# Kernel optimization log

Measured on AMD Instinct MI355X. Metric: run time of the kernel, lower is better.

The kernel has to match this reference:

```python
import jax, jax.numpy as jnp
import numpy as np

B, T, E, H, V = 64, 512, 512, 1024, 32000


def setup_inputs() -> dict:
    key = jax.random.key(0)
    k1, k2, k3, k4, k5 = jax.random.split(key, 5)
    scale = 1.0 / np.sqrt(H)
    return {
        "source": jax.random.randint(k1, (B, T), 0, V),
        "emb_table": jax.random.normal(k2, (V, E), dtype=jnp.float32),
        "W_ih": jax.random.normal(k3, (E, 4 * H), dtype=jnp.float32) * scale,
        "W_hh": jax.random.normal(k4, (H, 4 * H), dtype=jnp.float32) * scale,
        "b": jax.random.normal(k5, (4 * H,), dtype=jnp.float32) * scale,
    }


def reference(source, emb_table, W_ih, W_hh, b):
    # Embedding lookup: [B, T, E]
    embedded = emb_table[source]
    batch = source.shape[0]
    hidden = W_hh.shape[0]
    h0 = jnp.zeros((batch, hidden), dtype=emb_table.dtype)
    c0 = jnp.zeros((batch, hidden), dtype=emb_table.dtype)

    # Sequential LSTM cell loop over timesteps, expressed as lax.scan.
    xs = jnp.swapaxes(embedded, 0, 1)  # [T, B, E]

    def step(carry, x_t):
        h, c = carry
        z = x_t @ W_ih + h @ W_hh + b  # [B, 4H]
        i, f, g, o = jnp.split(z, 4, axis=-1)
        i = jax.nn.sigmoid(i)
        f = jax.nn.sigmoid(f)
        g = jnp.tanh(g)
        o = jax.nn.sigmoid(o)
        c_new = f * c + i * g
        h_new = o * jnp.tanh(c_new)
        return (h_new, c_new), None

    (h_T, c_T), _ = jax.lax.scan(step, (h0, c0), xs)
    return h_T, c_T
```

## Files before the change

### kernel.cpp

```cpp
#include <hip/hip_runtime.h>
#include <hip/hip_bf16.h>

#define TT 512
#define BB 64
#define EE 512
#define HH 1024

typedef __attribute__((ext_vector_type(8))) short short8;
typedef __attribute__((ext_vector_type(4))) float f32x4;

#define WS_X     0
#define WS_WT    33554432
#define WS_HBUF  46137344
#define WS_FLAGS 46399488
#define WS_PROBE 48496640

static __device__ __forceinline__ unsigned short f2bf(float x) {
    unsigned int u = __float_as_uint(x);
    unsigned int r = (u + 0x7fffu + ((u >> 16) & 1u)) >> 16;
    return (unsigned short)r;
}

static __device__ __forceinline__ int fl_ld(const int* p) {
    return __hip_atomic_load(p, __ATOMIC_RELAXED, __HIP_MEMORY_SCOPE_AGENT);
}
static __device__ __forceinline__ void fl_st(int* p, int v) {
    __hip_atomic_store(p, v, __ATOMIC_RELAXED, __HIP_MEMORY_SCOPE_AGENT);
}
static __device__ __forceinline__ void h_st(unsigned int* p, unsigned int v) {
    __hip_atomic_store(p, v, __ATOMIC_RELAXED, __HIP_MEMORY_SCOPE_AGENT);
}
static __device__ __forceinline__ short8 h_ld16(const unsigned long long* p) {
    union { short8 v; unsigned long long q[2]; } u;
    u.q[0] = __hip_atomic_load(p,     __ATOMIC_RELAXED, __HIP_MEMORY_SCOPE_AGENT);
    u.q[1] = __hip_atomic_load(p + 1, __ATOMIC_RELAXED, __HIP_MEMORY_SCOPE_AGENT);
    return u.v;
}

__global__ void embed_k(const int* __restrict__ src, const float* __restrict__ emb,
                        unsigned short* __restrict__ X) {
    int idx  = blockIdx.x * 256 + threadIdx.x;
    int base = idx * 4;
    int t = base >> 15;
    int r = base & 32767;
    int b = r >> 9;
    int e = r & 511;
    int v = src[b * TT + t];
    float4 f = *(const float4*)(emb + (size_t)v * EE + e);
    ushort4 s;
    s.x = f2bf(f.x); s.y = f2bf(f.y); s.z = f2bf(f.z); s.w = f2bf(f.w);
    *(ushort4*)(X + base) = s;
}

__global__ void wprep_k(const float* __restrict__ Wih, const float* __restrict__ Whh,
                        unsigned short* __restrict__ Wt, int* __restrict__ probe) {
    const int bid = blockIdx.x;
    const int kk  = bid % 48;
    const int ct  = bid / 48;
    const int tid = threadIdx.x;

    if (bid == 0 && tid == 0) {
        int xcd;
        asm volatile("s_getreg_b32 %0, hwreg(HW_REG_XCC_ID)" : "=s"(xcd));
        int* pr = probe;
        asm volatile("global_store_dword %0, %1, off sc0"
                     :: "v"(pr), "v"(xcd) : "memory");
        int v;
        asm volatile("global_load_dword %0, %1, off sc0\n\ts_waitcnt vmcnt(0)"
                     : "=v"(v) : "v"(pr) : "memory");
        pr[1] = v;
    }

    const int k0 = kk * 32, c0 = ct * 16;
    __shared__ float tile[32][17];
    for (int e = tid; e < 512; e += 256) {
        int kr = e >> 4, cc = e & 15;
        int k = k0 + kr;
        float v = (k < EE) ? Wih[(size_t)k * 4096 + c0 + cc]
                           : Whh[(size_t)(k - EE) * 4096 + c0 + cc];
        tile[kr][cc] = v;
    }
    __syncthreads();
    for (int e = tid; e < 512; e += 256) {
        int lane = e >> 3, j = e & 7;
        float v = tile[(lane >> 4) * 8 + j][lane & 15];
        Wt[(size_t)bid * 512 + e] = f2bf(v);
    }
}

__global__ __launch_bounds__(256, 1) void lstm_k(
    const unsigned short* __restrict__ X,
    const unsigned short* __restrict__ Wt,
    const float* __restrict__ bias,
    unsigned short* __restrict__ hbuf,
    int* __restrict__ flags,
    float* __restrict__ out)
{
    const int g        = blockIdx.x;
    const int cg       = g & 63;
    const int rg       = g >> 6;
    const int row_base = rg * 16;
    const int ubase    = cg * 16;
    const int tid  = threadIdx.x;
    const int wave = tid >> 6;
    const int lane = tid & 63;
    const int lrow = lane & 15;
    const int quad = lane >> 4;

    __shared__ float zred[4][4][16][17];
    __shared__ float sbias[64];

    if (tid < 64) sbias[tid] = bias[(tid >> 4) * HH + ubase + (tid & 15)];

    short8 wr[12][4];
#pragma unroll
    for (int i = 0; i < 12; ++i) {
        const int kk = i * 4 + wave;
#pragma unroll
        for (int g4 = 0; g4 < 4; ++g4) {
            const int ct = g4 * 64 + cg;
            wr[i][g4] = *(const short8*)(Wt + ((size_t)(ct * 48 + kk)) * 512 + lane * 8);
        }
    }

    const int erow = tid >> 4, eu = tid & 15;
    float creg = 0.f;
    __syncthreads();

    for (int t = 0; t < TT; ++t) {
        f32x4 acc0 = {0.f,0.f,0.f,0.f}, acc1 = {0.f,0.f,0.f,0.f};
        f32x4 acc2 = {0.f,0.f,0.f,0.f}, acc3 = {0.f,0.f,0.f,0.f};

        const unsigned short* xp = X + ((size_t)(t * BB) + row_base + lrow) * EE + quad * 8;
#pragma unroll
        for (int i = 0; i < 4; ++i) {
            const int kk = i * 4 + wave;
            short8 a = *(const short8*)(xp + kk * 32);
            acc0 = __builtin_amdgcn_mfma_f32_16x16x32_bf16(a, wr[i][0], acc0, 0, 0, 0);
            acc1 = __builtin_amdgcn_mfma_f32_16x16x32_bf16(a, wr[i][1], acc1, 0, 0, 0);
            acc2 = __builtin_amdgcn_mfma_f32_16x16x32_bf16(a, wr[i][2], acc2, 0, 0, 0);
            acc3 = __builtin_amdgcn_mfma_f32_16x16x32_bf16(a, wr[i][3], acc3, 0, 0, 0);
        }

        if (t > 0) {
            if (tid < 64) {
                const int* fp = &flags[(((t - 1) * 4 + rg) * 64 + tid) * 4];
                while (fl_ld(fp) == 0) { }
            }
            __syncthreads();
        }

        const unsigned long long* hq = (const unsigned long long*)hbuf
            + ((size_t)(((t & 1) ^ 1) * BB) + row_base + lrow) * (HH / 4) + quad * 2;
        short8 ah[8];
#pragma unroll
        for (int i = 0; i < 8; ++i) {
            const int kk = (i + 4) * 4 + wave;
            ah[i] = h_ld16(hq + (kk * 8 - 128));
        }
#pragma unroll
        for (int i = 0; i < 8; ++i) {
            acc0 = __builtin_amdgcn_mfma_f32_16x16x32_bf16(ah[i], wr[i + 4][0], acc0, 0, 0, 0);
            acc1 = __builtin_amdgcn_mfma_f32_16x16x32_bf16(ah[i], wr[i + 4][1], acc1, 0, 0, 0);
            acc2 = __builtin_amdgcn_mfma_f32_16x16x32_bf16(ah[i], wr[i + 4][2], acc2, 0, 0, 0);
            acc3 = __builtin_amdgcn_mfma_f32_16x16x32_bf16(ah[i], wr[i + 4][3], acc3, 0, 0, 0);
        }

#pragma unroll
        for (int r = 0; r < 4; ++r) {
            zred[wave][0][quad * 4 + r][lrow] = acc0[r];
            zred[wave][1][quad * 4 + r][lrow] = acc1[r];
            zred[wave][2][quad * 4 + r][lrow] = acc2[r];
            zred[wave][3][quad * 4 + r][lrow] = acc3[r];
        }
        __syncthreads();

        {
            float zi = zred[0][0][erow][eu] + zred[1][0][erow][eu]
                     + zred[2][0][erow][eu] + zred[3][0][erow][eu] + sbias[eu];
            float zf = zred[0][1][erow][eu] + zred[1][1][erow][eu]
                     + zred[2][1][erow][eu] + zred[3][1][erow][eu] + sbias[16 + eu];
            float zg = zred[0][2][erow][eu] + zred[1][2][erow][eu]
                     + zred[2][2][erow][eu] + zred[3][2][erow][eu] + sbias[32 + eu];
            float zo = zred[0][3][erow][eu] + zred[1][3][erow][eu]
                     + zred[2][3][erow][eu] + zred[3][3][erow][eu] + sbias[48 + eu];
            float iv = 1.f / (1.f + __expf(-zi));
            float fv = 1.f / (1.f + __expf(-zf));
            float gv = 1.f - 2.f / (__expf(2.f * zg) + 1.f);
            float ov = 1.f / (1.f + __expf(-zo));
            float c  = fv * creg + iv * gv;
            creg = c;
            float th = 1.f - 2.f / (__expf(2.f * c) + 1.f);
            float h  = ov * th;

            float hp = __shfl_xor(h, 1);
            if ((eu & 1) == 0) {
                unsigned int v = (unsigned int)f2bf(h)
                               | ((unsigned int)f2bf(hp) << 16);
                unsigned int* hw = (unsigned int*)hbuf;
                h_st(hw + ((size_t)(t & 1) * BB + row_base + erow) * (HH / 2)
                        + (ubase >> 1) + (eu >> 1), v);
            }
            if (t == TT - 1) {
                out[(row_base + erow) * HH + ubase + eu] = h;
                out[BB * HH + (row_base + erow) * HH + ubase + eu] = c;
            }
        }
        __syncthreads();

        if (tid == 0) {
            fl_st(&flags[((t * 4 + rg) * 64 + cg) * 4], 1);
        }
    }
}

extern "C" void kernel_launch(void* const* d_in, const int* in_sizes, int n_in,
                              void* d_out, int out_size, void* d_ws, size_t ws_size,
                              hipStream_t stream) {
    const int*   src  = (const int*)d_in[0];
    const float* emb  = (const float*)d_in[1];
    const float* Wih  = (const float*)d_in[2];
    const float* Whh  = (const float*)d_in[3];
    const float* bias = (const float*)d_in[4];
    float* out = (float*)d_out;

    char* ws = (char*)d_ws;
    unsigned short* X     = (unsigned short*)(ws + WS_X);
    unsigned short* Wt    = (unsigned short*)(ws + WS_WT);
    unsigned short* hbuf  = (unsigned short*)(ws + WS_HBUF);
    int*            flags = (int*)(ws + WS_FLAGS);
    int*            probe = (int*)(ws + WS_PROBE);

    hipMemsetAsync(hbuf, 0, 2 * BB * HH * 2, stream);
    hipMemsetAsync(flags, 0, TT * 4 * 64 * 4 * 4, stream);
    embed_k<<<dim3(16384), dim3(256), 0, stream>>>(src, emb, X);
    wprep_k<<<dim3(12288), dim3(256), 0, stream>>>(Wih, Whh, Wt, probe);
    lstm_k<<<dim3(256), dim3(256), 0, stream>>>(X, Wt, bias, hbuf, flags, out);
}
```

Baseline: 2.041 ms.

## Prefetch next-step inputs, vectorize h exchange, and spin-wait in every wave

The next timestep's x rows are prefetched with raw global loads after the cell update, so their latency overlaps the flag wait. The h state is now read with dwordx4 loads and written as 16-byte stores packed through lane shuffles, using sc0 sc1 cache bypass instead of atomic 8-byte and 4-byte accesses. Every wave now polls the flags itself with s_sleep, which removes a block barrier. Bias moves into registers and the __syncthreads calls become raw s_barrier with manual waitcnt. This shortens the per-step critical path of the recurrent loop, but memory ordering now depends on hand-placed waitcnt and cache bits, which is fragile.

```diff
diff --git a/kernel.cpp b/kernel.cpp
--- a/kernel.cpp
+++ b/kernel.cpp
@@ -8,6 +8,7 @@
 
 typedef __attribute__((ext_vector_type(8))) short short8;
 typedef __attribute__((ext_vector_type(4))) float f32x4;
+typedef __attribute__((ext_vector_type(4))) unsigned int u32x4;
 
 #define WS_X     0
 #define WS_WT    33554432
@@ -26,15 +27,6 @@
 }
 static __device__ __forceinline__ void fl_st(int* p, int v) {
     __hip_atomic_store(p, v, __ATOMIC_RELAXED, __HIP_MEMORY_SCOPE_AGENT);
-}
-static __device__ __forceinline__ void h_st(unsigned int* p, unsigned int v) {
-    __hip_atomic_store(p, v, __ATOMIC_RELAXED, __HIP_MEMORY_SCOPE_AGENT);
-}
-static __device__ __forceinline__ short8 h_ld16(const unsigned long long* p) {
-    union { short8 v; unsigned long long q[2]; } u;
-    u.q[0] = __hip_atomic_load(p,     __ATOMIC_RELAXED, __HIP_MEMORY_SCOPE_AGENT);
-    u.q[1] = __hip_atomic_load(p + 1, __ATOMIC_RELAXED, __HIP_MEMORY_SCOPE_AGENT);
-    return u.v;
 }
 
 __global__ void embed_k(const int* __restrict__ src, const float* __restrict__ emb,
@@ -106,11 +98,14 @@
     const int lane = tid & 63;
     const int lrow = lane & 15;
     const int quad = lane >> 4;
+    const int erow = tid >> 4, eu = tid & 15;
 
     __shared__ float zred[4][4][16][17];
-    __shared__ float sbias[64];
-
-    if (tid < 64) sbias[tid] = bias[(tid >> 4) * HH + ubase + (tid & 15)];
+
+    const float bi_ = bias[          ubase + eu];
+    const float bf_ = bias[HH      + ubase + eu];
+    const float bg_ = bias[2 * HH  + ubase + eu];
+    const float bo_ = bias[3 * HH  + ubase + eu];
 
     short8 wr[12][4];
 #pragma unroll
@@ -123,41 +118,51 @@
         }
     }
 
-    const int erow = tid >> 4, eu = tid & 15;
     float creg = 0.f;
-    __syncthreads();
+
+    short8 ax[4];
+    {
+        const unsigned short* xp = X + ((size_t)row_base + lrow) * EE + quad * 8;
+#pragma unroll
+        for (int i = 0; i < 4; ++i)
+            asm volatile("global_load_dwordx4 %0, %1, off"
+                         : "=v"(ax[i]) : "v"(xp + (i * 4 + wave) * 32) : "memory");
+    }
 
     for (int t = 0; t < TT; ++t) {
+        if (t > 0) {
+            const int* fp = &flags[(((t - 1) * 4 + rg) << 8) + (lane << 2)];
+            while (fl_ld(fp) == 0) { __builtin_amdgcn_s_sleep(1); }
+            asm volatile("s_waitcnt vmcnt(0)" ::: "memory");
+            __builtin_amdgcn_sched_barrier(0);
+        }
+
+        const unsigned short* hrow = hbuf
+            + ((size_t)(((t & 1) ^ 1) * BB) + row_base + lrow) * HH + quad * 8;
+        short8 ah[8];
+#pragma unroll
+        for (int i = 0; i < 8; ++i)
+            asm volatile("global_load_dwordx4 %0, %1, off sc0 sc1"
+                         : "=v"(ah[i])
+                         : "v"(hrow + (size_t)((i * 4 + wave) * 32)) : "memory");
+
+        asm volatile("s_waitcnt vmcnt(8)" ::: "memory");
+        __builtin_amdgcn_sched_barrier(0);
+
         f32x4 acc0 = {0.f,0.f,0.f,0.f}, acc1 = {0.f,0.f,0.f,0.f};
         f32x4 acc2 = {0.f,0.f,0.f,0.f}, acc3 = {0.f,0.f,0.f,0.f};
 
-        const unsigned short* xp = X + ((size_t)(t * BB) + row_base + lrow) * EE + quad * 8;
 #pragma unroll
         for (int i = 0; i < 4; ++i) {
-            const int kk = i * 4 + wave;
-            short8 a = *(const short8*)(xp + kk * 32);
-            acc0 = __builtin_amdgcn_mfma_f32_16x16x32_bf16(a, wr[i][0], acc0, 0, 0, 0);
-            acc1 = __builtin_amdgcn_mfma_f32_16x16x32_bf16(a, wr[i][1], acc1, 0, 0, 0);
-            acc2 = __builtin_amdgcn_mfma_f32_16x16x32_bf16(a, wr[i][2], acc2, 0, 0, 0);
-            acc3 = __builtin_amdgcn_mfma_f32_16x16x32_bf16(a, wr[i][3], acc3, 0, 0, 0);
-        }
-
-        if (t > 0) {
-            if (tid < 64) {
-                const int* fp = &flags[(((t - 1) * 4 + rg) * 64 + tid) * 4];
-                while (fl_ld(fp) == 0) { }
-            }
-            __syncthreads();
-        }
-
-        const unsigned long long* hq = (const unsigned long long*)hbuf
-            + ((size_t)(((t & 1) ^ 1) * BB) + row_base + lrow) * (HH / 4) + quad * 2;
-        short8 ah[8];
-#pragma unroll
-        for (int i = 0; i < 8; ++i) {
-            const int kk = (i + 4) * 4 + wave;
-            ah[i] = h_ld16(hq + (kk * 8 - 128));
-        }
+            acc0 = __builtin_amdgcn_mfma_f32_16x16x32_bf16(ax[i], wr[i][0], acc0, 0, 0, 0);
+            acc1 = __builtin_amdgcn_mfma_f32_16x16x32_bf16(ax[i], wr[i][1], acc1, 0, 0, 0);
+            acc2 = __builtin_amdgcn_mfma_f32_16x16x32_bf16(ax[i], wr[i][2], acc2, 0, 0, 0);
+            acc3 = __builtin_amdgcn_mfma_f32_16x16x32_bf16(ax[i], wr[i][3], acc3, 0, 0, 0);
+        }
+
+        asm volatile("s_waitcnt vmcnt(0)" ::: "memory");
+        __builtin_amdgcn_sched_barrier(0);
+
 #pragma unroll
         for (int i = 0; i < 8; ++i) {
             acc0 = __builtin_amdgcn_mfma_f32_16x16x32_bf16(ah[i], wr[i + 4][0], acc0, 0, 0, 0);
@@ -173,43 +178,54 @@
             zred[wave][2][quad * 4 + r][lrow] = acc2[r];
             zred[wave][3][quad * 4 + r][lrow] = acc3[r];
         }
-        __syncthreads();
-
-        {
-            float zi = zred[0][0][erow][eu] + zred[1][0][erow][eu]
-                     + zred[2][0][erow][eu] + zred[3][0][erow][eu] + sbias[eu];
-            float zf = zred[0][1][erow][eu] + zred[1][1][erow][eu]
-                     + zred[2][1][erow][eu] + zred[3][1][erow][eu] + sbias[16 + eu];
-            float zg = zred[0][2][erow][eu] + zred[1][2][erow][eu]
-                     + zred[2][2][erow][eu] + zred[3][2][erow][eu] + sbias[32 + eu];
-            float zo = zred[0][3][erow][eu] + zred[1][3][erow][eu]
-                     + zred[2][3][erow][eu] + zred[3][3][erow][eu] + sbias[48 + eu];
-            float iv = 1.f / (1.f + __expf(-zi));
-            float fv = 1.f / (1.f + __expf(-zf));
-            float gv = 1.f - 2.f / (__expf(2.f * zg) + 1.f);
-            float ov = 1.f / (1.f + __expf(-zo));
-            float c  = fv * creg + iv * gv;
-            creg = c;
-            float th = 1.f - 2.f / (__expf(2.f * c) + 1.f);
-            float h  = ov * th;
-
-            float hp = __shfl_xor(h, 1);
-            if ((eu & 1) == 0) {
-                unsigned int v = (unsigned int)f2bf(h)
-                               | ((unsigned int)f2bf(hp) << 16);
-                unsigned int* hw = (unsigned int*)hbuf;
-                h_st(hw + ((size_t)(t & 1) * BB + row_base + erow) * (HH / 2)
-                        + (ubase >> 1) + (eu >> 1), v);
+        asm volatile("s_waitcnt lgkmcnt(0)" ::: "memory");
+        asm volatile("s_barrier" ::: "memory");
+
+        float zi = zred[0][0][erow][eu] + zred[1][0][erow][eu]
+                 + zred[2][0][erow][eu] + zred[3][0][erow][eu] + bi_;
+        float zf = zred[0][1][erow][eu] + zred[1][1][erow][eu]
+                 + zred[2][1][erow][eu] + zred[3][1][erow][eu] + bf_;
+        float zg = zred[0][2][erow][eu] + zred[1][2][erow][eu]
+                 + zred[2][2][erow][eu] + zred[3][2][erow][eu] + bg_;
+        float zo = zred[0][3][erow][eu] + zred[1][3][erow][eu]
+                 + zred[2][3][erow][eu] + zred[3][3][erow][eu] + bo_;
+        float iv = 1.f / (1.f + __expf(-zi));
+        float fv = 1.f / (1.f + __expf(-zf));
+        float gv = 1.f - 2.f / (__expf(2.f * zg) + 1.f);
+        float ov = 1.f / (1.f + __expf(-zo));
+        float c  = fv * creg + iv * gv;
+        creg = c;
+        float th = 1.f - 2.f / (__expf(2.f * c) + 1.f);
+        float h  = ov * th;
+
+        if (t < TT - 1) {
+            float hp1 = __shfl_xor(h, 1);
+            unsigned int v01 = (unsigned int)f2bf(h) | ((unsigned int)f2bf(hp1) << 16);
+            unsigned int v23 = (unsigned int)__shfl_xor((int)v01, 2);
+            unsigned int v45 = (unsigned int)__shfl_xor((int)v01, 4);
+            unsigned int v67 = (unsigned int)__shfl_xor((int)v23, 4);
+            if ((eu & 7) == 0) {
+                u32x4 pk; pk.x = v01; pk.y = v23; pk.z = v45; pk.w = v67;
+                unsigned short* hw = hbuf + ((size_t)(t & 1) * BB + row_base + erow) * HH
+                                   + ubase + eu;
+                asm volatile("global_store_dwordx4 %0, %1, off sc0 sc1"
+                             :: "v"(hw), "v"(pk) : "memory");
             }
-            if (t == TT - 1) {
-                out[(row_base + erow) * HH + ubase + eu] = h;
-                out[BB * HH + (row_base + erow) * HH + ubase + eu] = c;
-            }
-        }
-        __syncthreads();
-
-        if (tid == 0) {
-            fl_st(&flags[((t * 4 + rg) * 64 + cg) * 4], 1);
+            const unsigned short* xp2 = X + ((size_t)((t + 1) * BB) + row_base + lrow) * EE
+                                      + quad * 8;
+#pragma unroll
+            for (int i = 0; i < 4; ++i)
+                asm volatile("global_load_dwordx4 %0, %1, off"
+                             : "=v"(ax[i]) : "v"(xp2 + (i * 4 + wave) * 32) : "memory");
+            asm volatile("s_waitcnt vmcnt(4)" ::: "memory");
+        } else {
+            out[(row_base + erow) * HH + ubase + eu] = h;
+            out[BB * HH + (row_base + erow) * HH + ubase + eu] = c;
+        }
+
+        asm volatile("s_barrier" ::: "memory");
+        if (t < TT - 1 && tid == 0) {
+            fl_st(&flags[((t * 4 + rg) << 8) + (cg << 2)], 1);
         }
     }
 }
```

New measurement: 2.436 ms. 19.4% more time.
